# Optimization experiments

Hardware: AMD Instinct MI355X
Metric: run time of the kernel (lower is better)

The kernel has to match this reference:

```python
import jax, jax.numpy as jnp
import numpy as np
import math

B, S, D, NH = 2, 2048, 1024, 16
DK = D // NH
E, TOPK, MOE_H, NSH = 8, 2, 1024, 2
SH_H = MOE_H * NSH
EPS = 1e-6


def setup_inputs() -> dict:
    key = jax.random.key(0)
    ks = jax.random.split(key, 24)
    p = lambda k, shape: jax.random.normal(k, shape, jnp.float32) * 0.02
    x = jax.random.normal(ks[0], (B, S, D), jnp.float32)
    # RoPE tables: freqs_cis = exp(i * t * theta^{-2j/dk}), passed as cos/sin
    inv = 1.0 / (10000.0 ** (np.arange(0, DK, 2, dtype=np.float32) / DK))
    ang = np.outer(np.arange(S, dtype=np.float32), inv)
    freqs_cos = jnp.asarray(np.cos(ang), jnp.float32)
    freqs_sin = jnp.asarray(np.sin(ang), jnp.float32)
    mask = jnp.triu(jnp.full((S, S), -1e9, jnp.float32), k=1)  # causal additive mask
    return {
        'x': x, 'freqs_cos': freqs_cos, 'freqs_sin': freqs_sin, 'mask': mask,
        'wq': p(ks[1], (D, D)), 'wk': p(ks[2], (D, D)),
        'wv': p(ks[3], (D, D)), 'wo': p(ks[4], (D, D)),
        'attn_norm_w': jnp.ones((D,), jnp.float32),
        'ffn_norm_w': jnp.ones((D,), jnp.float32),
        'gate_w': p(ks[5], (E, D)), 'gate_b': p(ks[6], (E,)),
        'w1': p(ks[7], (E, MOE_H, D)), 'b1': p(ks[8], (E, MOE_H)),
        'w2': p(ks[9], (E, D, MOE_H)), 'b2': p(ks[10], (E, D)),
        'w3': p(ks[11], (E, MOE_H, D)), 'b3': p(ks[12], (E, MOE_H)),
        'sg_w': p(ks[13], (SH_H, D)), 'su_w': p(ks[14], (SH_H, D)),
        'sd_w': p(ks[15], (D, SH_H)),
    }


def rmsnorm(x, w):
    f = x.astype(jnp.float32)
    y = f * jax.lax.rsqrt(jnp.mean(f * f, axis=-1, keepdims=True) + EPS)
    return y.astype(x.dtype) * w


def rope(t, cos, sin):
    # t: [b, s, h, dk]; pairs (t[2j], t[2j+1]) as complex, multiplied by e^{i ang}
    tr, ti = t[..., 0::2], t[..., 1::2]
    c, s = cos[None, :, None, :], sin[None, :, None, :]
    outr = tr * c - ti * s
    outi = tr * s + ti * c
    return jnp.stack([outr, outi], axis=-1).reshape(t.shape)


def reference(x, freqs_cos, freqs_sin, mask, wq, wk, wv, wo, attn_norm_w, ffn_norm_w,
              gate_w, gate_b, w1, b1, w2, b2, w3, b3, sg_w, su_w, sd_w):
    b, s, d = x.shape
    # --- attention with RoPE ---
    h = rmsnorm(x, attn_norm_w)
    q = (h @ wq.T).reshape(b, s, NH, DK)
    k = (h @ wk.T).reshape(b, s, NH, DK)
    v = (h @ wv.T).reshape(b, s, NH, DK)
    q = rope(q, freqs_cos, freqs_sin)
    k = rope(k, freqs_cos, freqs_sin)
    scale = 1.0 / math.sqrt(DK)
    q = q.transpose(0, 2, 1, 3)
    k = k.transpose(0, 2, 1, 3)
    v = v.transpose(0, 2, 1, 3)
    scores = jnp.einsum('bhqd,bhkd->bhqk', q, k) * scale + mask
    # NOTE: source divides by sqrt(d_k) a second time before softmax (faithful quirk)
    attn = jax.nn.softmax(scores * scale, axis=-1)
    o = jnp.einsum('bhqk,bhkd->bhqd', attn, v).transpose(0, 2, 1, 3).reshape(b, s, d)
    x = x + o @ wo.T
    # --- MoE FFN ---
    hf = rmsnorm(x, ffn_norm_w).reshape(-1, d)                 # [T, D]
    gscores = jax.nn.softmax(hf @ gate_w.T + gate_b, axis=-1)  # [T, E]
    _, idx = jax.lax.top_k(gscores, TOPK)                      # bias is None -> topk on scores
    weights = jnp.take_along_axis(gscores, idx, axis=1)        # original_scores gather
    wmask = (jax.nn.one_hot(idx, E, dtype=hf.dtype) * weights[..., None]).sum(1)  # [T, E]
    shared = (jax.nn.silu(hf @ sg_w.T) * (hf @ su_w.T)) @ sd_w.T
    a1 = jnp.einsum('td,ehd->teh', hf, w1) + b1
    a3 = jnp.einsum('td,ehd->teh', hf, w3) + b3
    eo = jnp.einsum('teh,edh->ted', jax.nn.silu(a1) * a3, w2) + b2  # [T, E, D]
    router = jnp.einsum('te,ted->td', wmask, eo)
    return x + (shared + router).reshape(x.shape)
```

## Files before the change

### kernel.cpp

```cpp
#include <hip/hip_runtime.h>


typedef unsigned short u16;
typedef __attribute__((ext_vector_type(8))) short bh8;
typedef __attribute__((ext_vector_type(4))) float fv4;
typedef __attribute__((ext_vector_type(4))) unsigned uv4;
typedef __attribute__((ext_vector_type(2))) int iv2;

#define LOG2E 1.4426950408889634f
#define MAX_TILES 71

__device__ __forceinline__ float b2f(u16 u) {
  return __builtin_bit_cast(float, ((unsigned)u) << 16);
}
__device__ __forceinline__ u16 f2b(float f) {
  unsigned x = __builtin_bit_cast(unsigned, f);
  return (u16)((x + 0x7fffu + ((x >> 16) & 1u)) >> 16);
}
__device__ __forceinline__ fv4 mfma16(bh8 a, bh8 b, fv4 c) {
  return __builtin_amdgcn_mfma_f32_16x16x32_bf16(a, b, c, 0, 0, 0);
}
__device__ __forceinline__ unsigned cvtpk(float lo, float hi) {
  unsigned r;
  asm("v_cvt_pk_bf16_f32 %0, %1, %2" : "=v"(r) : "v"(lo), "v"(hi));
  return r;
}

#define GLD16(g, l)                                                        \
  __builtin_amdgcn_global_load_lds(                                        \
      (const __attribute__((address_space(1))) void*)(g),                  \
      (__attribute__((address_space(3))) void*)(l), 16, 0, 0)

__device__ __forceinline__ bh8 lds_frag(const u16* base, int row, int b8) {
  int off = row * 128 + ((b8 * 16) ^ ((row & 7) << 4));
  return *(const bh8*)((const char*)base + off);
}

template <int MODE, int TM = 128>
__global__ __launch_bounds__(256) void gemm_bt(
    const u16* __restrict__ A, const u16* __restrict__ B, int M, int N, int K,
    u16* __restrict__ Cb, float* __restrict__ Cf,
    const float* __restrict__ add1, const float* __restrict__ add2,
    const float* __restrict__ bias, const int* __restrict__ tmeta,
    const int* __restrict__ etok) {
  constexpr int MR = TM / 32;
  __shared__ u16 As[TM * 64];
  __shared__ u16 Bs[128 * 64];
  const int lane = threadIdx.x & 63;
  const int wid = threadIdx.x >> 6;
  const int wr = wid >> 1, wc = wid & 1;
  const int n0 = blockIdx.x * 128;
  const int rr = lane >> 3;
  const int b8s = (lane & 7) ^ rr;
  const int ldA = (MODE == 6) ? M : K;

  int m0 = 0, e = 0, m0l = 0, cnt = 0, row0 = 0;
  const u16* Bp = B;
  if constexpr (MODE == 5 || MODE == 6) {
    int tile = blockIdx.y;
    if (tile >= tmeta[0]) return;
    e = tmeta[16 + tile * 4];
    m0l = tmeta[17 + tile * 4];
    cnt = tmeta[18 + tile * 4];
    row0 = tmeta[19 + tile * 4];
    Bp = B + (size_t)e * N * K;
  } else {
    m0 = blockIdx.y * TM;
  }

  const u16* Arow[MR];
  const u16* Brow[4];
#pragma unroll
  for (int i = 0; i < MR; ++i) {
    int c = wid * MR + i;
    int row = c * 8 + rr;
    if constexpr (MODE == 5) {
      int li = m0l + row;
      li = li < cnt ? li : cnt - 1;
      int tok = etok[e * 4096 + li];
      Arow[i] = A + (size_t)tok * ldA + b8s * 8;
    } else if constexpr (MODE == 6) {
      Arow[i] = A + (size_t)(row0 + row) * ldA + b8s * 8;
    } else {
      Arow[i] = A + (size_t)(m0 + row) * ldA + b8s * 8;
    }
  }
#pragma unroll
  for (int i = 0; i < 4; ++i)
    Brow[i] = Bp + (size_t)(n0 + (wid * 4 + i) * 8 + rr) * K + b8s * 8;

  fv4 acc[MR][4] = {};
  for (int k0 = 0; k0 < K; k0 += 64) {
    __syncthreads();
#pragma unroll
    for (int i = 0; i < MR; ++i)
      GLD16(Arow[i] + k0, &As[(wid * MR + i) * 512]);
#pragma unroll
    for (int i = 0; i < 4; ++i)
      GLD16(Brow[i] + k0, &Bs[(wid * 4 + i) * 512]);
    __syncthreads();
#pragma unroll
    for (int ks = 0; ks < 2; ++ks) {
      int b8 = ks * 4 + (lane >> 4);
      bh8 af[MR], bf[4];
#pragma unroll
      for (int mi = 0; mi < MR; ++mi)
        af[mi] = lds_frag(As, wr * (16 * MR) + mi * 16 + (lane & 15), b8);
#pragma unroll
      for (int ni = 0; ni < 4; ++ni)
        bf[ni] = lds_frag(Bs, wc * 64 + ni * 16 + (lane & 15), b8);
      __builtin_amdgcn_s_setprio(1);
#pragma unroll
      for (int mi = 0; mi < MR; ++mi)
#pragma unroll
        for (int ni = 0; ni < 4; ++ni)
          acc[mi][ni] = mfma16(af[mi], bf[ni], acc[mi][ni]);
      __builtin_amdgcn_s_setprio(0);
    }
  }

  const int rbase = (MODE == 5 || MODE == 6) ? row0 : m0;
  const int r0b = rbase + wr * (16 * MR) + (lane >> 4) * 4;
  const int c0b = n0 + wc * 64 + (lane & 15);
  const float* bb = nullptr;
  if constexpr (MODE == 6) bb = bias + (size_t)e * N;
#pragma unroll
  for (int mi = 0; mi < MR; ++mi) {
#pragma unroll
    for (int ni = 0; ni < 4; ++ni) {
      int c = c0b + ni * 16;
#pragma unroll
      for (int r = 0; r < 4; ++r) {
        int row = r0b + mi * 16 + r;
        size_t idx = (size_t)row * N + c;
        float v = acc[mi][ni][r];
        if constexpr (MODE == 0) Cb[idx] = f2b(v);
        else if constexpr (MODE == 1) Cf[idx] = add1[idx] + v;
        else if constexpr (MODE == 4) Cf[idx] = add1[idx] + add2[idx] + v;
        else if constexpr (MODE == 5) Cb[idx] = f2b(v);
        else Cb[idx] = f2b(v + bb[c]);
      }
    }
  }
}

__global__ __launch_bounds__(256) void rmsnorm_bf16(
    const float* __restrict__ x, const float* __restrict__ w,
    u16* __restrict__ out) {
  int t = blockIdx.x;
  const float* xr = x + (size_t)t * 1024;
  fv4 v = *(const fv4*)(xr + threadIdx.x * 4);
  float ss = v[0] * v[0] + v[1] * v[1] + v[2] * v[2] + v[3] * v[3];
#pragma unroll
  for (int off = 1; off < 64; off <<= 1) ss += __shfl_xor(ss, off);
  __shared__ float red[4];
  int lane = threadIdx.x & 63, wid = threadIdx.x >> 6;
  if (lane == 0) red[wid] = ss;
  __syncthreads();
  float inv = rsqrtf((red[0] + red[1] + red[2] + red[3]) * (1.0f / 1024.f) + 1e-6f);
  u16* op = out + (size_t)t * 1024 + threadIdx.x * 4;
  const float* wp = w + threadIdx.x * 4;
#pragma unroll
  for (int i = 0; i < 4; ++i) op[i] = f2b(v[i] * inv * wp[i]);
}

__global__ __launch_bounds__(256) void rope_repack(
    const u16* __restrict__ qkv, const float* __restrict__ fc,
    const float* __restrict__ fs, u16* __restrict__ qr, u16* __restrict__ kr,
    u16* __restrict__ vt, int S) {
  __shared__ u16 tile[64][65];
  const int s0 = blockIdx.x * 64;
  const int b = blockIdx.y;
  const int h0 = blockIdx.z * 4;
#pragma unroll 4
  for (int it = 0; it < 32; ++it) {
    int idx = threadIdx.x + it * 256;
    int tl = idx >> 7, rem = idx & 127;
    int h = h0 + (rem >> 5), i = rem & 31;
    int s = s0 + tl;
    float c = fc[s * 32 + i], sn = fs[s * 32 + i];
    size_t src = ((size_t)(b * S + s)) * 3072 + h * 64 + 2 * i;
    size_t dst = ((size_t)((b * 16 + h) * S + s)) * 64 + 2 * i;
    float a0 = b2f(qkv[src]), a1 = b2f(qkv[src + 1]);
    qr[dst] = f2b(a0 * c - a1 * sn);
    qr[dst + 1] = f2b(a0 * sn + a1 * c);
    float b0 = b2f(qkv[src + 1024]), b1 = b2f(qkv[src + 1025]);
    kr[dst] = f2b(b0 * c - b1 * sn);
    kr[dst + 1] = f2b(b0 * sn + b1 * c);
  }
  for (int hh = 0; hh < 4; ++hh) {
    int h = h0 + hh;
    __syncthreads();
    for (int cc = threadIdx.x; cc < 512; cc += 256) {
      int tl = cc >> 3, d8 = cc & 7;
      bh8 val = *(const bh8*)(qkv + ((size_t)(b * S + s0 + tl)) * 3072 + 2048 +
                              h * 64 + d8 * 8);
#pragma unroll
      for (int j = 0; j < 8; ++j) tile[tl][d8 * 8 + j] = (u16)val[j];
    }
    __syncthreads();
    for (int cc = threadIdx.x; cc < 512; cc += 256) {
      int d = cc >> 3, pg = cc & 7;
      int sbase = 16 * (pg >> 2) + 4 * (pg & 3);
      bh8 o;
#pragma unroll
      for (int j = 0; j < 8; ++j)
        o[j] = (short)tile[sbase + (j & 3) + ((j >> 2) << 5)][d];
      *(bh8*)(vt + ((size_t)((b * 16 + h) * 64 + d)) * S + s0 + pg * 8) = o;
    }
  }
}

__global__ __launch_bounds__(256) void attn_fwd(
    const u16* __restrict__ qr, const u16* __restrict__ kr,
    const u16* __restrict__ vt, u16* __restrict__ ob, int S, int NHc) {
  __shared__ u16 Ks[2][64 * 64];
  __shared__ u16 Vs[2][64 * 64];
  const int lane = threadIdx.x & 63;
  const int wid = threadIdx.x >> 6;
  const int g = lane >> 4;
  const int l15 = lane & 15;
  const int bh = blockIdx.x;
  const int ia = blockIdx.y;
  const int nq = S / 64;
  const int qa0 = ia * 64;
  const int qb0 = (nq - 1 - ia) * 64;
  const int b = bh / NHc, h = bh % NHc;
  const u16* qbase = qr + (size_t)bh * S * 64;
  const u16* kb = kr + (size_t)bh * S * 64;
  const u16* vb = vt + (size_t)bh * 64 * S;
  const float SC = 0.015625f * LOG2E;
  const int rr = lane >> 3;
  const int b8s = (lane & 7) ^ rr;

  bh8 qfA[2], qfB[2];
  {
    const u16* qp = qbase + (size_t)(qa0 + wid * 16 + l15) * 64 + g * 8;
    qfA[0] = *(const bh8*)qp;
    qfA[1] = *(const bh8*)(qp + 32);
    qp = qbase + (size_t)(qb0 + wid * 16 + l15) * 64 + g * 8;
    qfB[0] = *(const bh8*)qp;
    qfB[1] = *(const bh8*)(qp + 32);
  }
  fv4 oaccA[4] = {}, oaccB[4] = {};
  float mA = -1e30f, lA = 0.f, mB = -1e30f, lB = 0.f;
  const int nktB = nq - ia;

  auto stage = [&](int buf, int j0) {
#pragma unroll
    for (int i = 0; i < 2; ++i) {
      int c = wid * 2 + i;
      int row = c * 8 + rr;
      GLD16(kb + (size_t)(j0 + row) * 64 + b8s * 8, &Ks[buf][c * 512]);
      GLD16(vb + (size_t)row * S + j0 + b8s * 8, &Vs[buf][c * 512]);
    }
  };
  stage(0, 0);

  auto process = [&](const u16* Kc, const u16* Vc, int j0, int q0x, bh8* qf,
                     fv4* oacc, float& mrow, float& lrow) {
    const int q_my = q0x + wid * 16 + l15;
    fv4 st[4] = {};
    __builtin_amdgcn_s_setprio(1);
#pragma unroll
    for (int ks = 0; ks < 2; ++ks) {
      int b8 = ks * 4 + g;
#pragma unroll
      for (int jt = 0; jt < 4; ++jt) {
        bh8 kf = lds_frag(Kc, jt * 16 + l15, b8);
        st[jt] = mfma16(kf, qf[ks], st[jt]);
      }
    }
    __builtin_amdgcn_s_setprio(0);

    float p[4][4];
    float mloc = -1e30f;
    const int jb = j0 + 4 * g;
    if (j0 + 63 > q0x + wid * 16) {
#pragma unroll
      for (int jt = 0; jt < 4; ++jt)
#pragma unroll
        for (int r = 0; r < 4; ++r) {
          int j = jb + jt * 16 + r;
          float s = st[jt][r] * SC;
          s = (j <= q_my) ? s : -1e30f;
          p[jt][r] = s;
          mloc = fmaxf(mloc, s);
        }
    } else {
#pragma unroll
      for (int jt = 0; jt < 4; ++jt)
#pragma unroll
        for (int r = 0; r < 4; ++r) {
          float s = st[jt][r] * SC;
          p[jt][r] = s;
          mloc = fmaxf(mloc, s);
        }
    }
    mloc = fmaxf(mloc, __shfl_xor(mloc, 16));
    mloc = fmaxf(mloc, __shfl_xor(mloc, 32));
    bool defer = __all(mloc <= mrow + 8.f);
    float sfac = 1.f;
    if (!defer) {
      float mnew = fmaxf(mrow, mloc);
      sfac = exp2f(mrow - mnew);
      mrow = mnew;
    }
    float rsum = 0.f;
#pragma unroll
    for (int jt = 0; jt < 4; ++jt)
#pragma unroll
      for (int r = 0; r < 4; ++r) {
        float pv = exp2f(p[jt][r] - mrow);
        p[jt][r] = pv;
        rsum += pv;
      }
    rsum += __shfl_xor(rsum, 16);
    rsum += __shfl_xor(rsum, 32);
    lrow = lrow * sfac + rsum;
    if (!defer) {
      float sf[4];
#pragma unroll
      for (int r = 0; r < 4; ++r) sf[r] = __shfl(sfac, g * 4 + r);
#pragma unroll
      for (int dt = 0; dt < 4; ++dt)
#pragma unroll
        for (int r = 0; r < 4; ++r) oacc[dt][r] *= sf[r];
    }

    __builtin_amdgcn_s_setprio(1);
#pragma unroll
    for (int ks = 0; ks < 2; ++ks) {
      uv4 w;
      w[0] = cvtpk(p[ks][0], p[ks][1]);
      w[1] = cvtpk(p[ks][2], p[ks][3]);
      w[2] = cvtpk(p[ks + 2][0], p[ks + 2][1]);
      w[3] = cvtpk(p[ks + 2][2], p[ks + 2][3]);
      bh8 pa = __builtin_bit_cast(bh8, w);
#pragma unroll
      for (int dt = 0; dt < 4; ++dt) {
        bh8 vf = lds_frag(Vc, dt * 16 + l15, ks * 4 + g);
        oacc[dt] = mfma16(pa, vf, oacc[dt]);
      }
    }
    __builtin_amdgcn_s_setprio(0);
  };

  for (int kt = 0; kt < nktB; ++kt) {
    const int j0 = kt * 64;
    __syncthreads();
    if (kt + 1 < nktB) stage((kt + 1) & 1, (kt + 1) * 64);
    const u16* Kc = Ks[kt & 1];
    const u16* Vc = Vs[kt & 1];
    process(Kc, Vc, j0, qb0, qfB, oaccB, mB, lB);
    if (kt <= ia) process(Kc, Vc, j0, qa0, qfA, oaccA, mA, lA);
  }

  auto wout = [&](fv4* oacc, float lrow, int q0x) {
    float lr[4];
#pragma unroll
    for (int r = 0; r < 4; ++r) lr[r] = __shfl(lrow, g * 4 + r);
#pragma unroll
    for (int dt = 0; dt < 4; ++dt)
#pragma unroll
      for (int r = 0; r < 4; ++r) {
        int row = q0x + wid * 16 + g * 4 + r;
        int col = dt * 16 + l15;
        ob[((size_t)b * S + row) * 1024 + h * 64 + col] =
            f2b(oacc[dt][r] / lr[r]);
      }
  };
  wout(oaccA, lA, qa0);
  wout(oaccB, lB, qb0);
}

__global__ __launch_bounds__(256) void gate_topk(
    const float* __restrict__ x2, const float* __restrict__ nw,
    const float* __restrict__ gw, const float* __restrict__ gb,
    int* __restrict__ topk_e, float* __restrict__ topk_w) {
  int t = blockIdx.x * 4 + (threadIdx.x >> 6);
  int lane = threadIdx.x & 63;
  const float* xr = x2 + (size_t)t * 1024;
  float hv[16];
  float ss = 0.f;
#pragma unroll
  for (int i = 0; i < 4; ++i) {
    fv4 v = *(const fv4*)(xr + lane * 16 + i * 4);
#pragma unroll
    for (int j = 0; j < 4; ++j) {
      hv[i * 4 + j] = v[j];
      ss += v[j] * v[j];
    }
  }
#pragma unroll
  for (int off = 1; off < 64; off <<= 1) ss += __shfl_xor(ss, off);
  float inv = rsqrtf(ss * (1.0f / 1024.f) + 1e-6f);
  const fv4* nwp = (const fv4*)(nw + lane * 16);
#pragma unroll
  for (int i = 0; i < 4; ++i) {
    fv4 wv = nwp[i];
#pragma unroll
    for (int j = 0; j < 4; ++j) hv[i * 4 + j] *= inv * wv[j];
  }
  float logit[8];
#pragma unroll
  for (int e = 0; e < 8; ++e) {
    const fv4* wp = (const fv4*)(gw + (size_t)e * 1024 + lane * 16);
    float s = 0.f;
#pragma unroll
    for (int i = 0; i < 4; ++i) {
      fv4 wv = wp[i];
#pragma unroll
      for (int j = 0; j < 4; ++j) s += hv[i * 4 + j] * wv[j];
    }
    logit[e] = s;
  }
#pragma unroll
  for (int off = 1; off < 64; off <<= 1)
#pragma unroll
    for (int e = 0; e < 8; ++e) logit[e] += __shfl_xor(logit[e], off);
  if (lane == 0) {
#pragma unroll
    for (int e = 0; e < 8; ++e) logit[e] += gb[e];
    float mx = logit[0];
#pragma unroll
    for (int e = 1; e < 8; ++e) mx = fmaxf(mx, logit[e]);
    float pe[8], se = 0.f;
#pragma unroll
    for (int e = 0; e < 8; ++e) { pe[e] = __expf(logit[e] - mx); se += pe[e]; }
    float rs = 1.f / se;
#pragma unroll
    for (int e = 0; e < 8; ++e) pe[e] *= rs;
    int i0 = 0;
    float b0 = pe[0];
#pragma unroll
    for (int e = 1; e < 8; ++e)
      if (pe[e] > b0) { b0 = pe[e]; i0 = e; }
    int i1 = -1;
    float b1v = -1.f;
#pragma unroll
    for (int e = 0; e < 8; ++e)
      if (e != i0 && pe[e] > b1v) { b1v = pe[e]; i1 = e; }
    topk_e[2 * t] = i0;
    topk_e[2 * t + 1] = i1;
    topk_w[2 * t] = b0;
    topk_w[2 * t + 1] = b1v;
  }
}

__global__ __launch_bounds__(512) void scatter_tokens(
    const int* __restrict__ topk_e, int* __restrict__ counts,
    int* __restrict__ pos_of, int* __restrict__ etok, int T2) {
  const int e = threadIdx.x >> 6;
  const int lane = threadIdx.x & 63;
  int base = 0;
  for (int i0 = 0; i0 < T2; i0 += 128) {
    iv2 te = *(const iv2*)(topk_e + i0 + lane * 2);
    unsigned long long m0 = __ballot(te[0] == e);
    unsigned long long m1 = __ballot(te[1] == e);
    unsigned long long lt = (1ull << lane) - 1;
    int pre = __popcll(m0 & lt) + __popcll(m1 & lt);
    if (te[0] == e) {
      int pos = base + pre;
      etok[e * 4096 + pos] = (i0 >> 1) + lane;
      pos_of[i0 + lane * 2] = pos;
      ++pre;
    }
    if (te[1] == e) {
      int pos = base + pre;
      etok[e * 4096 + pos] = (i0 >> 1) + lane;
      pos_of[i0 + lane * 2 + 1] = pos;
    }
    base += __popcll(m0) + __popcll(m1);
  }
  if (lane == 0) counts[e] = base;
}

__global__ __launch_bounds__(256) void sched_moe(const int* __restrict__ counts,
                                                 int* __restrict__ meta,
                                                 int* __restrict__ rexp) {
  __shared__ int s_e[MAX_TILES], s_row0[MAX_TILES], s_tt, s_rb;
  if (threadIdx.x == 0) {
    int tt = 0, rb = 0;
    for (int e = 0; e < 8; ++e) {
      meta[1 + e] = rb;
      int c = counts[e];
      int nt = (c + 127) >> 7;
      for (int i = 0; i < nt; ++i) {
        meta[16 + tt * 4] = e;
        meta[17 + tt * 4] = i * 128;
        meta[18 + tt * 4] = c;
        meta[19 + tt * 4] = rb + i * 128;
        s_e[tt] = e;
        s_row0[tt] = rb + i * 128;
        ++tt;
      }
      rb += nt * 128;
    }
    meta[0] = tt;
    s_tt = tt;
    s_rb = rb;
  }
  __syncthreads();
  int tt = s_tt;
  for (int tile = 0; tile < tt; ++tile) {
    int r0 = s_row0[tile], e = s_e[tile];
    for (int j = threadIdx.x; j < 128; j += 256) rexp[r0 + j] = e;
  }
  for (int r = s_rb + threadIdx.x; r < MAX_TILES * 128; r += 256) rexp[r] = 0;
}

__global__ __launch_bounds__(256) void silu_moe(
    u16* __restrict__ a13, const float* __restrict__ b1,
    const float* __restrict__ b3, const int* __restrict__ rexp) {
  size_t i = ((size_t)blockIdx.x * 256 + threadIdx.x) * 8;
  int row = (int)(i >> 10), col = (int)(i & 1023);
  int e = rexp[row];
  const float* ba = b1 + (size_t)e * 1024 + col;
  const float* bb = b3 + (size_t)e * 1024 + col;
  u16* rp = a13 + (size_t)row * 2048 + col;
  bh8 av = *(const bh8*)rp;
  bh8 bv = *(const bh8*)(rp + 1024);
  bh8 ov;
#pragma unroll
  for (int j = 0; j < 8; ++j) {
    float x = b2f((u16)av[j]) + ba[j];
    float y = b2f((u16)bv[j]) + bb[j];
    float s = x / (1.f + __expf(-x));
    ov[j] = (short)f2b(s * y);
  }
  *(bh8*)rp = ov;
}

__global__ __launch_bounds__(128) void combine_router(
    const u16* __restrict__ eo, const int* __restrict__ topk_e,
    const float* __restrict__ topk_w, const int* __restrict__ pos_of,
    const int* __restrict__ meta, float* __restrict__ router) {
  int t = blockIdx.x;
  int c = threadIdx.x * 8;
  int e0 = topk_e[2 * t], e1 = topk_e[2 * t + 1];
  float w0 = topk_w[2 * t], w1 = topk_w[2 * t + 1];
  int r0 = meta[1 + e0] + pos_of[2 * t];
  int r1 = meta[1 + e1] + pos_of[2 * t + 1];
  bh8 v0 = *(const bh8*)(eo + (size_t)r0 * 1024 + c);
  bh8 v1 = *(const bh8*)(eo + (size_t)r1 * 1024 + c);
  float* rp = router + (size_t)t * 1024 + c;
#pragma unroll
  for (int j = 0; j < 8; ++j)
    rp[j] = w0 * b2f((u16)v0[j]) + w1 * b2f((u16)v1[j]);
}

__global__ __launch_bounds__(256) void silu_sh(const u16* __restrict__ sgu,
                                               u16* __restrict__ hs) {
  size_t i = ((size_t)blockIdx.x * 256 + threadIdx.x) * 8;
  size_t row = i >> 11, col = i & 2047;
  const u16* rp = sgu + row * 4096 + col;
  bh8 av = *(const bh8*)rp;
  bh8 bv = *(const bh8*)(rp + 2048);
  bh8 ov;
#pragma unroll
  for (int j = 0; j < 8; ++j) {
    float x = b2f((u16)av[j]);
    float y = b2f((u16)bv[j]);
    float s = x / (1.f + __expf(-x));
    ov[j] = (short)f2b(s * y);
  }
  *(bh8*)(hs + i) = ov;
}

__global__ __launch_bounds__(256) void f2b_convert(
    const float* __restrict__ src, u16* __restrict__ dst) {
  size_t i = ((size_t)blockIdx.x * 256 + threadIdx.x) * 8;
  fv4 a = *(const fv4*)(src + i);
  fv4 b = *(const fv4*)(src + i + 4);
  bh8 o;
#pragma unroll
  for (int j = 0; j < 4; ++j) o[j] = (short)f2b(a[j]);
#pragma unroll
  for (int j = 0; j < 4; ++j) o[4 + j] = (short)f2b(b[j]);
  *(bh8*)(dst + i) = o;
}

__global__ __launch_bounds__(256) void f2b_convert_moe(
    const float* __restrict__ src, u16* __restrict__ dst, int halfoff) {
  size_t i = ((size_t)blockIdx.x * 256 + threadIdx.x) * 8;
  size_t e = i >> 20, inner = i & 1048575;
  fv4 a = *(const fv4*)(src + i);
  fv4 b = *(const fv4*)(src + i + 4);
  bh8 o;
#pragma unroll
  for (int j = 0; j < 4; ++j) o[j] = (short)f2b(a[j]);
#pragma unroll
  for (int j = 0; j < 4; ++j) o[4 + j] = (short)f2b(b[j]);
  *(bh8*)(dst + e * 2097152 + halfoff + inner) = o;
}

extern "C" void kernel_launch(void* const* d_in, const int* in_sizes, int n_in,
                              void* d_out, int out_size, void* d_ws,
                              size_t ws_size, hipStream_t stream) {
  (void)in_sizes; (void)n_in; (void)out_size; (void)ws_size;
  const int Sc = 2048, Dc = 1024, NHc = 16, Tc = 4096, SH = 2048;

  const float* x   = (const float*)d_in[0];
  const float* fc  = (const float*)d_in[1];
  const float* fs  = (const float*)d_in[2];
  const float* wq  = (const float*)d_in[4];
  const float* wk  = (const float*)d_in[5];
  const float* wv  = (const float*)d_in[6];
  const float* wo  = (const float*)d_in[7];
  const float* anw = (const float*)d_in[8];
  const float* fnw = (const float*)d_in[9];
  const float* gw  = (const float*)d_in[10];
  const float* gb  = (const float*)d_in[11];
  const float* w1  = (const float*)d_in[12];
  const float* b1  = (const float*)d_in[13];
  const float* w2  = (const float*)d_in[14];
  const float* b2  = (const float*)d_in[15];
  const float* w3  = (const float*)d_in[16];
  const float* b3  = (const float*)d_in[17];
  const float* sgw = (const float*)d_in[18];
  const float* suw = (const float*)d_in[19];
  const float* sdw = (const float*)d_in[20];
  float* out = (float*)d_out;

  char* base = (char*)d_ws;
  size_t off = 0;
  auto alloc = [&](size_t bytes) -> void* {
    void* p = base + off;
    off += (bytes + 255) & ~(size_t)255;
    return p;
  };
  u16* wqkv_b = (u16*)alloc(2ull * 3072 * 1024);
  u16* wo_b   = (u16*)alloc(2ull * 1024 * 1024);
  u16* sgu_b  = (u16*)alloc(2ull * 4096 * 1024);
  u16* sdw_b  = (u16*)alloc(2ull * 1024 * 2048);
  u16* w13_b  = (u16*)alloc(2ull * 8 * 2048 * 1024);
  u16* w2_b   = (u16*)alloc(2ull * 8 * 1024 * 1024);
  char* regA = (char*)alloc(2ull * Tc * 4096);
  char* regB = (char*)alloc(2ull * (size_t)MAX_TILES * 128 * 2048);
  float* x2  = (float*)alloc(4ull * Tc * Dc);
  u16* hs_b  = (u16*)alloc(2ull * Tc * SH);
  int* counts = (int*)alloc(8 * 4);
  int* topk_e = (int*)alloc(2ull * Tc * 4);
  float* topk_w = (float*)alloc(2ull * Tc * 4);
  int* pos_of = (int*)alloc(2ull * Tc * 4);
  int* etok = (int*)alloc(8ull * 4096 * 4);
  int* meta = (int*)alloc(512 * 4);
  int* rexp = (int*)alloc((size_t)MAX_TILES * 128 * 4);

  u16* qkv_out = (u16*)regA;
  u16* sgu_out = (u16*)regA;
  u16* eo_c    = (u16*)regA;
  u16* h_b  = (u16*)regB;
  u16* qr   = (u16*)regB;
  u16* kr   = (u16*)(regB + 2ull * Tc * Dc);
  u16* vt_  = (u16*)(regB + 4ull * Tc * Dc);
  u16* o_b  = (u16*)(regB + 6ull * Tc * Dc);
  u16* a13_c = (u16*)regB;
  float* router = (float*)regB;
  u16* hf_b = wqkv_b;

  auto conv = [&](const float* s, u16* d, size_t n) {
    f2b_convert<<<dim3((unsigned)(n / 2048)), 256, 0, stream>>>(s, d);
  };
  conv(wq, wqkv_b, (size_t)Dc * Dc);
  conv(wk, wqkv_b + 1048576, (size_t)Dc * Dc);
  conv(wv, wqkv_b + 2097152, (size_t)Dc * Dc);
  conv(wo, wo_b, (size_t)Dc * Dc);
  conv(sgw, sgu_b, (size_t)SH * Dc);
  conv(suw, sgu_b + 2097152, (size_t)SH * Dc);
  conv(sdw, sdw_b, (size_t)Dc * SH);
  conv(w2, w2_b, 8ull * 1024 * 1024);
  f2b_convert_moe<<<4096, 256, 0, stream>>>(w1, w13_b, 0);
  f2b_convert_moe<<<4096, 256, 0, stream>>>(w3, w13_b, 1048576);

  rmsnorm_bf16<<<Tc, 256, 0, stream>>>(x, anw, h_b);
  gemm_bt<0><<<dim3(3072 / 128, Tc / 128), 256, 0, stream>>>(
      h_b, wqkv_b, Tc, 3072, Dc, qkv_out, nullptr, nullptr, nullptr, nullptr,
      nullptr, nullptr);
  rope_repack<<<dim3(Sc / 64, 2, 4), 256, 0, stream>>>(qkv_out, fc, fs, qr, kr,
                                                       vt_, Sc);
  attn_fwd<<<dim3(2 * NHc, Sc / 128), 256, 0, stream>>>(qr, kr, vt_, o_b, Sc,
                                                        NHc);
  gemm_bt<1, 64><<<dim3(Dc / 128, Tc / 64), 256, 0, stream>>>(
      o_b, wo_b, Tc, Dc, Dc, nullptr, x2, x, nullptr, nullptr, nullptr,
      nullptr);

  rmsnorm_bf16<<<Tc, 256, 0, stream>>>(x2, fnw, hf_b);
  gate_topk<<<Tc / 4, 256, 0, stream>>>(x2, fnw, gw, gb, topk_e, topk_w);
  scatter_tokens<<<1, 512, 0, stream>>>(topk_e, counts, pos_of, etok, 2 * Tc);
  sched_moe<<<1, 256, 0, stream>>>(counts, meta, rexp);

  gemm_bt<0><<<dim3(4096 / 128, Tc / 128), 256, 0, stream>>>(
      hf_b, sgu_b, Tc, 4096, Dc, sgu_out, nullptr, nullptr, nullptr, nullptr,
      nullptr, nullptr);
  silu_sh<<<dim3((unsigned)(((size_t)Tc * SH) / 2048)), 256, 0, stream>>>(
      sgu_out, hs_b);

  gemm_bt<5><<<dim3(2048 / 128, MAX_TILES), 256, 0, stream>>>(
      hf_b, w13_b, Tc, 2048, Dc, a13_c, nullptr, nullptr, nullptr, nullptr,
      meta, etok);
  silu_moe<<<dim3((unsigned)(((size_t)MAX_TILES * 128 * 1024) / 2048)), 256, 0,
             stream>>>(a13_c, b1, b3, rexp);
  gemm_bt<6><<<dim3(Dc / 128, MAX_TILES), 256, 0, stream>>>(
      a13_c, w2_b, 2048, Dc, 1024, eo_c, nullptr, nullptr, nullptr,
      b2, meta, etok);
  combine_router<<<Tc, 128, 0, stream>>>(eo_c, topk_e, topk_w, pos_of, meta,
                                         router);

  gemm_bt<4, 64><<<dim3(Dc / 128, Tc / 64), 256, 0, stream>>>(
      hs_b, sdw_b, Tc, Dc, SH, nullptr, out, x2, router, nullptr, nullptr,
      nullptr);
}
```

Before: 444.3 us.

## Fuse SiLU-gating into GEMM epilogues, merge routing kernels, restructure attention softmax

Interleaves the gate and up weight rows in 32-row chunks during bf16 conversion, so each GEMM tile holds matching gate and up columns and the epilogue can apply bias, SiLU and the product directly. This removes the separate silu_sh and silu_moe passes and the full-width intermediate writes and reads. It also merges scatter_tokens and sched_moe into one route_tokens kernel, which drops the rexp table. In attention, K and V fragments are loaded once per tile and shared by both query blocks, the row sum is computed with an MFMA against a ones vector, and the scale multiply is folded into the exp2 argument. These changes raise register pressure and rely on the interleaved weight layout matching the epilogue indexing.

Measured after the change: 426.2 us. -4.1%, faster.

```diff
diff --git a/kernel.cpp b/kernel.cpp
--- a/kernel.cpp
+++ b/kernel.cpp
@@ -56,7 +56,7 @@
 
   int m0 = 0, e = 0, m0l = 0, cnt = 0, row0 = 0;
   const u16* Bp = B;
-  if constexpr (MODE == 5 || MODE == 6) {
+  if constexpr (MODE == 6 || MODE == 8) {
     int tile = blockIdx.y;
     if (tile >= tmeta[0]) return;
     e = tmeta[16 + tile * 4];
@@ -74,7 +74,7 @@
   for (int i = 0; i < MR; ++i) {
     int c = wid * MR + i;
     int row = c * 8 + rr;
-    if constexpr (MODE == 5) {
+    if constexpr (MODE == 8) {
       int li = m0l + row;
       li = li < cnt ? li : cnt - 1;
       int tok = etok[e * 4096 + li];
@@ -119,26 +119,56 @@
     }
   }
 
-  const int rbase = (MODE == 5 || MODE == 6) ? row0 : m0;
+  const int rbase = (MODE == 6 || MODE == 8) ? row0 : m0;
   const int r0b = rbase + wr * (16 * MR) + (lane >> 4) * 4;
-  const int c0b = n0 + wc * 64 + (lane & 15);
-  const float* bb = nullptr;
-  if constexpr (MODE == 6) bb = bias + (size_t)e * N;
-#pragma unroll
-  for (int mi = 0; mi < MR; ++mi) {
-#pragma unroll
-    for (int ni = 0; ni < 4; ++ni) {
-      int c = c0b + ni * 16;
-#pragma unroll
-      for (int r = 0; r < 4; ++r) {
-        int row = r0b + mi * 16 + r;
-        size_t idx = (size_t)row * N + c;
-        float v = acc[mi][ni][r];
-        if constexpr (MODE == 0) Cb[idx] = f2b(v);
-        else if constexpr (MODE == 1) Cf[idx] = add1[idx] + v;
-        else if constexpr (MODE == 4) Cf[idx] = add1[idx] + add2[idx] + v;
-        else if constexpr (MODE == 5) Cb[idx] = f2b(v);
-        else Cb[idx] = f2b(v + bb[c]);
+
+  if constexpr (MODE == 7 || MODE == 8) {
+    const int OUTN = N >> 1;
+    const int colb = (n0 >> 1) + wc * 32;
+    const float* bb1 = nullptr;
+    const float* bb3 = nullptr;
+    if constexpr (MODE == 8) {
+      bb1 = add1 + (size_t)e * OUTN;
+      bb3 = add2 + (size_t)e * OUTN;
+    }
+#pragma unroll
+    for (int mi = 0; mi < MR; ++mi) {
+#pragma unroll
+      for (int ni = 0; ni < 2; ++ni) {
+        int c = colb + ni * 16 + (lane & 15);
+#pragma unroll
+        for (int r = 0; r < 4; ++r) {
+          int row = r0b + mi * 16 + r;
+          float xg = acc[mi][ni][r];
+          float yu = acc[mi][ni + 2][r];
+          if constexpr (MODE == 8) {
+            xg += bb1[c];
+            yu += bb3[c];
+          }
+          float s = xg / (1.f + __expf(-xg));
+          Cb[(size_t)row * OUTN + c] = f2b(s * yu);
+        }
+      }
+    }
+  } else {
+    const int c0b = n0 + wc * 64 + (lane & 15);
+    const float* bb = nullptr;
+    if constexpr (MODE == 6) bb = bias + (size_t)e * N;
+#pragma unroll
+    for (int mi = 0; mi < MR; ++mi) {
+#pragma unroll
+      for (int ni = 0; ni < 4; ++ni) {
+        int c = c0b + ni * 16;
+#pragma unroll
+        for (int r = 0; r < 4; ++r) {
+          int row = r0b + mi * 16 + r;
+          size_t idx = (size_t)row * N + c;
+          float v = acc[mi][ni][r];
+          if constexpr (MODE == 0) Cb[idx] = f2b(v);
+          else if constexpr (MODE == 1) Cf[idx] = add1[idx] + v;
+          else if constexpr (MODE == 4) Cf[idx] = add1[idx] + add2[idx] + v;
+          else Cb[idx] = f2b(v + bb[c]);
+        }
       }
     }
   }
@@ -233,6 +263,10 @@
   const int rr = lane >> 3;
   const int b8s = (lane & 7) ^ rr;
 
+  bh8 ONES;
+#pragma unroll
+  for (int j = 0; j < 8; ++j) ONES[j] = (short)0x3f80;
+
   bh8 qfA[2], qfB[2];
   {
     const u16* qp = qbase + (size_t)(qa0 + wid * 16 + l15) * 64 + g * 8;
@@ -243,7 +277,8 @@
     qfB[1] = *(const bh8*)(qp + 32);
   }
   fv4 oaccA[4] = {}, oaccB[4] = {};
-  float mA = -1e30f, lA = 0.f, mB = -1e30f, lB = 0.f;
+  fv4 lA = {}, lB = {};
+  float mA = -1e30f, mB = -1e30f;
   const int nktB = nq - ia;
 
   auto stage = [&](int buf, int j0) {
@@ -257,23 +292,19 @@
   };
   stage(0, 0);
 
-  auto process = [&](const u16* Kc, const u16* Vc, int j0, int q0x, bh8* qf,
-                     fv4* oacc, float& mrow, float& lrow) {
+  auto process = [&](const bh8 (&kf)[2][4], const bh8 (&vf)[2][4], int j0,
+                     int q0x, bh8* qf, fv4* oacc, float& mrow, fv4& lrowC) {
     const int q_my = q0x + wid * 16 + l15;
     fv4 st[4] = {};
     __builtin_amdgcn_s_setprio(1);
 #pragma unroll
-    for (int ks = 0; ks < 2; ++ks) {
-      int b8 = ks * 4 + g;
-#pragma unroll
-      for (int jt = 0; jt < 4; ++jt) {
-        bh8 kf = lds_frag(Kc, jt * 16 + l15, b8);
-        st[jt] = mfma16(kf, qf[ks], st[jt]);
-      }
-    }
+    for (int ks = 0; ks < 2; ++ks)
+#pragma unroll
+      for (int jt = 0; jt < 4; ++jt)
+        st[jt] = mfma16(kf[ks][jt], qf[ks], st[jt]);
     __builtin_amdgcn_s_setprio(0);
 
-    float p[4][4];
+    float sr[4][4];
     float mloc = -1e30f;
     const int jb = j0 + 4 * g;
     if (j0 + 63 > q0x + wid * 16) {
@@ -282,9 +313,8 @@
 #pragma unroll
         for (int r = 0; r < 4; ++r) {
           int j = jb + jt * 16 + r;
-          float s = st[jt][r] * SC;
-          s = (j <= q_my) ? s : -1e30f;
-          p[jt][r] = s;
+          float s = (j <= q_my) ? st[jt][r] : -1e30f;
+          sr[jt][r] = s;
           mloc = fmaxf(mloc, s);
         }
     } else {
@@ -292,43 +322,37 @@
       for (int jt = 0; jt < 4; ++jt)
 #pragma unroll
         for (int r = 0; r < 4; ++r) {
-          float s = st[jt][r] * SC;
-          p[jt][r] = s;
-          mloc = fmaxf(mloc, s);
+          sr[jt][r] = st[jt][r];
+          mloc = fmaxf(mloc, st[jt][r]);
         }
     }
     mloc = fmaxf(mloc, __shfl_xor(mloc, 16));
     mloc = fmaxf(mloc, __shfl_xor(mloc, 32));
+    mloc *= SC;
     bool defer = __all(mloc <= mrow + 8.f);
-    float sfac = 1.f;
     if (!defer) {
       float mnew = fmaxf(mrow, mloc);
-      sfac = exp2f(mrow - mnew);
+      float sfac = exp2f(mrow - mnew);
       mrow = mnew;
-    }
-    float rsum = 0.f;
+      float sfC[4];
+#pragma unroll
+      for (int r = 0; r < 4; ++r) sfC[r] = __shfl(sfac, g * 4 + r);
+#pragma unroll
+      for (int dt = 0; dt < 4; ++dt)
+#pragma unroll
+        for (int r = 0; r < 4; ++r) oacc[dt][r] *= sfC[r];
+#pragma unroll
+      for (int r = 0; r < 4; ++r) lrowC[r] *= sfC[r];
+    }
+    float p[4][4];
 #pragma unroll
     for (int jt = 0; jt < 4; ++jt)
 #pragma unroll
-      for (int r = 0; r < 4; ++r) {
-        float pv = exp2f(p[jt][r] - mrow);
-        p[jt][r] = pv;
-        rsum += pv;
-      }
-    rsum += __shfl_xor(rsum, 16);
-    rsum += __shfl_xor(rsum, 32);
-    lrow = lrow * sfac + rsum;
-    if (!defer) {
-      float sf[4];
-#pragma unroll
-      for (int r = 0; r < 4; ++r) sf[r] = __shfl(sfac, g * 4 + r);
-#pragma unroll
-      for (int dt = 0; dt < 4; ++dt)
-#pragma unroll
-        for (int r = 0; r < 4; ++r) oacc[dt][r] *= sf[r];
-    }
+      for (int r = 0; r < 4; ++r)
+        p[jt][r] = exp2f(fmaf(sr[jt][r], SC, -mrow));
 
     __builtin_amdgcn_s_setprio(1);
+    fv4 racc = {};
 #pragma unroll
     for (int ks = 0; ks < 2; ++ks) {
       uv4 w;
@@ -337,13 +361,14 @@
       w[2] = cvtpk(p[ks + 2][0], p[ks + 2][1]);
       w[3] = cvtpk(p[ks + 2][2], p[ks + 2][3]);
       bh8 pa = __builtin_bit_cast(bh8, w);
-#pragma unroll
-      for (int dt = 0; dt < 4; ++dt) {
-        bh8 vf = lds_frag(Vc, dt * 16 + l15, ks * 4 + g);
-        oacc[dt] = mfma16(pa, vf, oacc[dt]);
-      }
+      racc = mfma16(pa, ONES, racc);
+#pragma unroll
+      for (int dt = 0; dt < 4; ++dt)
+        oacc[dt] = mfma16(pa, vf[ks][dt], oacc[dt]);
     }
     __builtin_amdgcn_s_setprio(0);
+#pragma unroll
+    for (int r = 0; r < 4; ++r) lrowC[r] += racc[r];
   };
 
   for (int kt = 0; kt < nktB; ++kt) {
@@ -352,14 +377,22 @@
     if (kt + 1 < nktB) stage((kt + 1) & 1, (kt + 1) * 64);
     const u16* Kc = Ks[kt & 1];
     const u16* Vc = Vs[kt & 1];
-    process(Kc, Vc, j0, qb0, qfB, oaccB, mB, lB);
-    if (kt <= ia) process(Kc, Vc, j0, qa0, qfA, oaccA, mA, lA);
-  }
-
-  auto wout = [&](fv4* oacc, float lrow, int q0x) {
-    float lr[4];
-#pragma unroll
-    for (int r = 0; r < 4; ++r) lr[r] = __shfl(lrow, g * 4 + r);
+    bh8 kf[2][4], vf[2][4];
+#pragma unroll
+    for (int ks = 0; ks < 2; ++ks) {
+      int b8 = ks * 4 + g;
+#pragma unroll
+      for (int jt = 0; jt < 4; ++jt)
+        kf[ks][jt] = lds_frag(Kc, jt * 16 + l15, b8);
+#pragma unroll
+      for (int dt = 0; dt < 4; ++dt)
+        vf[ks][dt] = lds_frag(Vc, dt * 16 + l15, b8);
+    }
+    process(kf, vf, j0, qb0, qfB, oaccB, mB, lB);
+    if (kt <= ia) process(kf, vf, j0, qa0, qfA, oaccA, mA, lA);
+  }
+
+  auto wout = [&](fv4* oacc, fv4 lrowC, int q0x) {
 #pragma unroll
     for (int dt = 0; dt < 4; ++dt)
 #pragma unroll
@@ -367,7 +400,7 @@
         int row = q0x + wid * 16 + g * 4 + r;
         int col = dt * 16 + l15;
         ob[((size_t)b * S + row) * 1024 + h * 64 + col] =
-            f2b(oacc[dt][r] / lr[r]);
+            f2b(oacc[dt][r] / lrowC[r]);
       }
   };
   wout(oaccA, lA, qa0);
@@ -448,9 +481,10 @@
   }
 }
 
-__global__ __launch_bounds__(512) void scatter_tokens(
-    const int* __restrict__ topk_e, int* __restrict__ counts,
-    int* __restrict__ pos_of, int* __restrict__ etok, int T2) {
+__global__ __launch_bounds__(512) void route_tokens(
+    const int* __restrict__ topk_e, int* __restrict__ pos_of,
+    int* __restrict__ etok, int* __restrict__ meta, int T2) {
+  __shared__ int scnt[8];
   const int e = threadIdx.x >> 6;
   const int lane = threadIdx.x & 63;
   int base = 0;
@@ -473,63 +507,26 @@
     }
     base += __popcll(m0) + __popcll(m1);
   }
-  if (lane == 0) counts[e] = base;
-}
-
-__global__ __launch_bounds__(256) void sched_moe(const int* __restrict__ counts,
-                                                 int* __restrict__ meta,
-                                                 int* __restrict__ rexp) {
-  __shared__ int s_e[MAX_TILES], s_row0[MAX_TILES], s_tt, s_rb;
+  if (lane == 0) scnt[e] = base;
+  __syncthreads();
   if (threadIdx.x == 0) {
     int tt = 0, rb = 0;
-    for (int e = 0; e < 8; ++e) {
-      meta[1 + e] = rb;
-      int c = counts[e];
+#pragma unroll
+    for (int e2 = 0; e2 < 8; ++e2) {
+      meta[1 + e2] = rb;
+      int c = scnt[e2];
       int nt = (c + 127) >> 7;
       for (int i = 0; i < nt; ++i) {
-        meta[16 + tt * 4] = e;
+        meta[16 + tt * 4] = e2;
         meta[17 + tt * 4] = i * 128;
         meta[18 + tt * 4] = c;
         meta[19 + tt * 4] = rb + i * 128;
-        s_e[tt] = e;
-        s_row0[tt] = rb + i * 128;
         ++tt;
       }
       rb += nt * 128;
     }
     meta[0] = tt;
-    s_tt = tt;
-    s_rb = rb;
-  }
-  __syncthreads();
-  int tt = s_tt;
-  for (int tile = 0; tile < tt; ++tile) {
-    int r0 = s_row0[tile], e = s_e[tile];
-    for (int j = threadIdx.x; j < 128; j += 256) rexp[r0 + j] = e;
-  }
-  for (int r = s_rb + threadIdx.x; r < MAX_TILES * 128; r += 256) rexp[r] = 0;
-}
-
-__global__ __launch_bounds__(256) void silu_moe(
-    u16* __restrict__ a13, const float* __restrict__ b1,
-    const float* __restrict__ b3, const int* __restrict__ rexp) {
-  size_t i = ((size_t)blockIdx.x * 256 + threadIdx.x) * 8;
-  int row = (int)(i >> 10), col = (int)(i & 1023);
-  int e = rexp[row];
-  const float* ba = b1 + (size_t)e * 1024 + col;
-  const float* bb = b3 + (size_t)e * 1024 + col;
-  u16* rp = a13 + (size_t)row * 2048 + col;
-  bh8 av = *(const bh8*)rp;
-  bh8 bv = *(const bh8*)(rp + 1024);
-  bh8 ov;
-#pragma unroll
-  for (int j = 0; j < 8; ++j) {
-    float x = b2f((u16)av[j]) + ba[j];
-    float y = b2f((u16)bv[j]) + bb[j];
-    float s = x / (1.f + __expf(-x));
-    ov[j] = (short)f2b(s * y);
-  }
-  *(bh8*)rp = ov;
+  }
 }
 
 __global__ __launch_bounds__(128) void combine_router(
@@ -550,24 +547,6 @@
     rp[j] = w0 * b2f((u16)v0[j]) + w1 * b2f((u16)v1[j]);
 }
 
-__global__ __launch_bounds__(256) void silu_sh(const u16* __restrict__ sgu,
-                                               u16* __restrict__ hs) {
-  size_t i = ((size_t)blockIdx.x * 256 + threadIdx.x) * 8;
-  size_t row = i >> 11, col = i & 2047;
-  const u16* rp = sgu + row * 4096 + col;
-  bh8 av = *(const bh8*)rp;
-  bh8 bv = *(const bh8*)(rp + 2048);
-  bh8 ov;
-#pragma unroll
-  for (int j = 0; j < 8; ++j) {
-    float x = b2f((u16)av[j]);
-    float y = b2f((u16)bv[j]);
-    float s = x / (1.f + __expf(-x));
-    ov[j] = (short)f2b(s * y);
-  }
-  *(bh8*)(hs + i) = ov;
-}
-
 __global__ __launch_bounds__(256) void f2b_convert(
     const float* __restrict__ src, u16* __restrict__ dst) {
   size_t i = ((size_t)blockIdx.x * 256 + threadIdx.x) * 8;
@@ -581,10 +560,14 @@
   *(bh8*)(dst + i) = o;
 }
 
-__global__ __launch_bounds__(256) void f2b_convert_moe(
-    const float* __restrict__ src, u16* __restrict__ dst, int halfoff) {
+__global__ __launch_bounds__(256) void f2b_convert_ilv(
+    const float* __restrict__ src, u16* __restrict__ dst, int half,
+    int seg_shift) {
   size_t i = ((size_t)blockIdx.x * 256 + threadIdx.x) * 8;
-  size_t e = i >> 20, inner = i & 1048575;
+  int r = (int)(i >> 10), col = (int)(i & 1023);
+  int rl = r & ((1 << seg_shift) - 1), e = r >> seg_shift;
+  int dstrow = (e << (seg_shift + 1)) + ((rl >> 5) << 6) + (rl & 31) +
+               (half << 5);
   fv4 a = *(const fv4*)(src + i);
   fv4 b = *(const fv4*)(src + i + 4);
   bh8 o;
@@ -592,7 +575,7 @@
   for (int j = 0; j < 4; ++j) o[j] = (short)f2b(a[j]);
 #pragma unroll
   for (int j = 0; j < 4; ++j) o[4 + j] = (short)f2b(b[j]);
-  *(bh8*)(dst + e * 2097152 + halfoff + inner) = o;
+  *(bh8*)(dst + (size_t)dstrow * 1024 + col) = o;
 }
 
 extern "C" void kernel_launch(void* const* d_in, const int* in_sizes, int n_in,
@@ -640,16 +623,13 @@
   char* regB = (char*)alloc(2ull * (size_t)MAX_TILES * 128 * 2048);
   float* x2  = (float*)alloc(4ull * Tc * Dc);
   u16* hs_b  = (u16*)alloc(2ull * Tc * SH);
-  int* counts = (int*)alloc(8 * 4);
   int* topk_e = (int*)alloc(2ull * Tc * 4);
   float* topk_w = (float*)alloc(2ull * Tc * 4);
   int* pos_of = (int*)alloc(2ull * Tc * 4);
   int* etok = (int*)alloc(8ull * 4096 * 4);
   int* meta = (int*)alloc(512 * 4);
-  int* rexp = (int*)alloc((size_t)MAX_TILES * 128 * 4);
 
   u16* qkv_out = (u16*)regA;
-  u16* sgu_out = (u16*)regA;
   u16* eo_c    = (u16*)regA;
   u16* h_b  = (u16*)regB;
   u16* qr   = (u16*)regB;
@@ -667,12 +647,12 @@
   conv(wk, wqkv_b + 1048576, (size_t)Dc * Dc);
   conv(wv, wqkv_b + 2097152, (size_t)Dc * Dc);
   conv(wo, wo_b, (size_t)Dc * Dc);
-  conv(sgw, sgu_b, (size_t)SH * Dc);
-  conv(suw, sgu_b + 2097152, (size_t)SH * Dc);
   conv(sdw, sdw_b, (size_t)Dc * SH);
   conv(w2, w2_b, 8ull * 1024 * 1024);
-  f2b_convert_moe<<<4096, 256, 0, stream>>>(w1, w13_b, 0);
-  f2b_convert_moe<<<4096, 256, 0, stream>>>(w3, w13_b, 1048576);
+  f2b_convert_ilv<<<1024, 256, 0, stream>>>(sgw, sgu_b, 0, 11);
+  f2b_convert_ilv<<<1024, 256, 0, stream>>>(suw, sgu_b, 1, 11);
+  f2b_convert_ilv<<<4096, 256, 0, stream>>>(w1, w13_b, 0, 10);
+  f2b_convert_ilv<<<4096, 256, 0, stream>>>(w3, w13_b, 1, 10);
 
   rmsnorm_bf16<<<Tc, 256, 0, stream>>>(x, anw, h_b);
   gemm_bt<0><<<dim3(3072 / 128, Tc / 128), 256, 0, stream>>>(
@@ -688,22 +668,16 @@
 
   rmsnorm_bf16<<<Tc, 256, 0, stream>>>(x2, fnw, hf_b);
   gate_topk<<<Tc / 4, 256, 0, stream>>>(x2, fnw, gw, gb, topk_e, topk_w);
-  scatter_tokens<<<1, 512, 0, stream>>>(topk_e, counts, pos_of, etok, 2 * Tc);
-  sched_moe<<<1, 256, 0, stream>>>(counts, meta, rexp);
-
-  gemm_bt<0><<<dim3(4096 / 128, Tc / 128), 256, 0, stream>>>(
-      hf_b, sgu_b, Tc, 4096, Dc, sgu_out, nullptr, nullptr, nullptr, nullptr,
+  route_tokens<<<1, 512, 0, stream>>>(topk_e, pos_of, etok, meta, 2 * Tc);
+
+  gemm_bt<7><<<dim3(4096 / 128, Tc / 128), 256, 0, stream>>>(
+      hf_b, sgu_b, Tc, 4096, Dc, hs_b, nullptr, nullptr, nullptr, nullptr,
       nullptr, nullptr);
-  silu_sh<<<dim3((unsigned)(((size_t)Tc * SH) / 2048)), 256, 0, stream>>>(
-      sgu_out, hs_b);
-
-  gemm_bt<5><<<dim3(2048 / 128, MAX_TILES), 256, 0, stream>>>(
-      hf_b, w13_b, Tc, 2048, Dc, a13_c, nullptr, nullptr, nullptr, nullptr,
-      meta, etok);
-  silu_moe<<<dim3((unsigned)(((size_t)MAX_TILES * 128 * 1024) / 2048)), 256, 0,
-             stream>>>(a13_c, b1, b3, rexp);
+
+  gemm_bt<8><<<dim3(2048 / 128, MAX_TILES), 256, 0, stream>>>(
+      hf_b, w13_b, Tc, 2048, Dc, a13_c, nullptr, b1, b3, nullptr, meta, etok);
   gemm_bt<6><<<dim3(Dc / 128, MAX_TILES), 256, 0, stream>>>(
-      a13_c, w2_b, 2048, Dc, 1024, eo_c, nullptr, nullptr, nullptr,
+      a13_c, w2_b, 1024, Dc, 1024, eo_c, nullptr, nullptr, nullptr,
       b2, meta, etok);
   combine_router<<<Tc, 128, 0, stream>>>(eo_c, topk_e, topk_w, pos_of, meta,
                                          router);
```
